# Performance work log

Measured on AMD Instinct MI355X. Metric: run time of the kernel, lower is better.

## Reference

```python
import jax, jax.numpy as jnp
import numpy as np

B, M, K, E, V, HOPS = 256, 128, 4, 512, 32000, 3


def setup_inputs() -> dict:
    key = jax.random.key(0)
    ks = jax.random.split(key, 12)

    def emb_table(k):
        t = 0.1 * jax.random.normal(k, (V, E), dtype=jnp.float32)
        return t.at[0].set(0.0)  # padding_idx=0

    inp = {
        "context": jax.random.randint(ks[0], (B, M, K), 0, V),
        "y_": jax.random.randint(ks[1], (B,), 0, V),
        "h_": jax.random.normal(ks[2], (1, B, E), dtype=jnp.float32),
        # embedding tables; C[i] tied to A[i+1], so distinct: A0,A1,A2,C2
        "A0": emb_table(ks[3]),
        "A1": emb_table(ks[4]),
        "A2": emb_table(ks[5]),
        "C2": emb_table(ks[6]),
        # GRU (single layer, single step): PyTorch layout [3E, E] and [3E]
        "W_ih": 0.05 * jax.random.normal(ks[7], (3 * E, E), dtype=jnp.float32),
        "W_hh": 0.05 * jax.random.normal(ks[8], (3 * E, E), dtype=jnp.float32),
        "b_ih": jnp.zeros((3 * E,), dtype=jnp.float32),
        "b_hh": jnp.zeros((3 * E,), dtype=jnp.float32),
        # lin_vocab: Linear(2E -> V)
        "lin_W": 0.02 * jax.random.normal(ks[9], (V, 2 * E), dtype=jnp.float32),
        "lin_b": jnp.zeros((V,), dtype=jnp.float32),
    }
    return inp


def _gru_step(x, h, W_ih, W_hh, b_ih, b_hh):
    gi = x @ W_ih.T + b_ih  # [B, 3E]
    gh = h @ W_hh.T + b_hh
    i_r, i_z, i_n = jnp.split(gi, 3, axis=-1)
    h_r, h_z, h_n = jnp.split(gh, 3, axis=-1)
    r = jax.nn.sigmoid(i_r + h_r)
    z = jax.nn.sigmoid(i_z + h_z)
    n = jnp.tanh(i_n + r * h_n)
    return (1.0 - z) * n + z * h


def reference(context, y_, h_, A0, A1, A2, C2, W_ih, W_hh, b_ih, b_hh, lin_W, lin_b):
    # memories[hop] = sum_k A[hop][context], memories[hops] = sum_k C[hops-1][context]
    tables = [A0, A1, A2, C2]
    memories = [t[context].sum(axis=2) for t in tables]  # each [B, M, E]

    m = A1[y_]  # C[0](y_) -- C[0].weight tied to A[1].weight, [B, E]
    h = _gru_step(m, h_[0], W_ih, W_hh, b_ih, b_hh)  # [B, E]

    q = h
    p = None
    p_vocab = None
    for hop in range(HOPS):
        p = jnp.einsum("bme,be->bm", memories[hop], q)  # dot-attention scores
        attn = jax.nn.softmax(p, axis=1)
        o = jnp.einsum("bm,bme->be", attn, memories[hop + 1])
        if hop == 0:
            p_vocab = jnp.concatenate([q, o], axis=1) @ lin_W.T + lin_b  # [B, V]
        q = q + o

    p_ptr = p  # last hop's pre-softmax scores [B, M]
    return (p_ptr, p_vocab, h[None])  # h: [1, B, E]
```

## Files before the change

kernel.cpp:

```cpp
#include <hip/hip_runtime.h>
#include <hip/hip_bf16.h>
#include <stdint.h>
#include <stddef.h>

#define Bb 256
#define Mm 128
#define Ee 512
#define Vv 32000
#define E3 1536

typedef __attribute__((ext_vector_type(8))) short bf16x8;
typedef __attribute__((ext_vector_type(4))) float f32x4;

__device__ __forceinline__ float bf2f(unsigned short u) {
  union { unsigned int i; float f; } v; v.i = ((unsigned int)u) << 16; return v.f;
}
__device__ __forceinline__ unsigned int f2bf(float f) {
  union { float f; unsigned int u; } v; v.f = f;
  unsigned int u = v.u;
  return ((u + 0x7fffu + ((u >> 16) & 1u)) >> 16);
}

__global__ void convert_kernel(const float* __restrict__ A0, const float* __restrict__ A1,
                               const float* __restrict__ A2,
                               unsigned short* __restrict__ tabB) {
  const int t = blockIdx.y;
  const float* src = (t == 0) ? A0 : (t == 1) ? A1 : A2;
  unsigned short* dst = tabB + (size_t)t * Vv * Ee;
  const int n4 = Vv * Ee / 4;
  for (int i = blockIdx.x * blockDim.x + threadIdx.x; i < n4; i += gridDim.x * blockDim.x) {
    f32x4 v = __builtin_nontemporal_load((const f32x4*)src + i);
    unsigned int o0 = f2bf(v.x) | (f2bf(v.y) << 16);
    unsigned int o1 = f2bf(v.z) | (f2bf(v.w) << 16);
    ((uint2*)dst)[i] = make_uint2(o0, o1);
  }
}

__global__ void gru_gemm_kernel(const int* __restrict__ y,
                                const float* __restrict__ A1,
                                const float* __restrict__ hprev,
                                const float* __restrict__ W_ih,
                                const float* __restrict__ W_hh,
                                float* __restrict__ gi,
                                float* __restrict__ gh) {
  const int z = blockIdx.z;
  const float* W = z ? W_hh : W_ih;
  float* C = z ? gh : gi;
  const int by = blockIdx.x * 64;
  const int jy = blockIdx.y * 64;
  __shared__ float As[16][65];
  __shared__ float Bs[16][65];
  const int tx = threadIdx.x & 15, ty = threadIdx.x >> 4;
  float acc[4][4] = {};
  for (int k0 = 0; k0 < Ee; k0 += 16) {
#pragma unroll
    for (int it = 0; it < 4; ++it) {
      int r = ty + it * 16;
      int row = by + r;
      const float* arow = z ? (hprev + (size_t)row * Ee) : (A1 + (size_t)y[row] * Ee);
      As[tx][r] = arow[k0 + tx];
      Bs[tx][r] = W[(size_t)(jy + r) * Ee + k0 + tx];
    }
    __syncthreads();
#pragma unroll
    for (int kk = 0; kk < 16; ++kk) {
      float a[4], bb[4];
#pragma unroll
      for (int i = 0; i < 4; ++i) { a[i] = As[kk][ty * 4 + i]; bb[i] = Bs[kk][tx * 4 + i]; }
#pragma unroll
      for (int i = 0; i < 4; ++i)
#pragma unroll
        for (int j = 0; j < 4; ++j)
          acc[i][j] += a[i] * bb[j];
    }
    __syncthreads();
  }
#pragma unroll
  for (int i = 0; i < 4; ++i)
#pragma unroll
    for (int j = 0; j < 4; ++j)
      C[(size_t)(by + ty * 4 + i) * E3 + jy + tx * 4 + j] = acc[i][j];
}

__global__ __launch_bounds__(1024) void fused_kernel(
    const int* __restrict__ ctx,
    const unsigned short* __restrict__ tabB,
    const float* __restrict__ A0, const float* __restrict__ A1,
    const float* __restrict__ A2,
    const float* __restrict__ gi, const float* __restrict__ gh,
    const float* __restrict__ b_ih, const float* __restrict__ b_hh,
    const float* __restrict__ h0,
    float* __restrict__ out_h, unsigned short* __restrict__ in2,
    float* __restrict__ p_out) {
  extern __shared__ char smem[];
  unsigned short* Vlds = (unsigned short*)smem;
  float* p_lds = (float*)(smem + 131072);
  float* qbuf = (float*)(smem + 131584);
  float* obuf = (float*)(smem + 133632);

  const int b = blockIdx.x;
  const int tid = threadIdx.x;
  const int lane = tid & 63, w = tid >> 6;

  if (tid < 512) {
    const int e = tid;
    const float* gib = gi + (size_t)b * E3;
    const float* ghb = gh + (size_t)b * E3;
    float ir = gib[e] + b_ih[e];
    float iz = gib[512 + e] + b_ih[512 + e];
    float inn = gib[1024 + e] + b_ih[1024 + e];
    float hr = ghb[e] + b_hh[e];
    float hz = ghb[512 + e] + b_hh[512 + e];
    float hn = ghb[1024 + e] + b_hh[1024 + e];
    float r = 1.f / (1.f + __expf(-(ir + hr)));
    float z = 1.f / (1.f + __expf(-(iz + hz)));
    float n = tanhf(inn + r * hn);
    float hp = h0[(size_t)b * Ee + e];
    float hnew = (1.f - z) * n + z * hp;
    out_h[(size_t)b * Ee + e] = hnew;
    in2[(size_t)b * 1024 + e] = (unsigned short)f2bf(hnew);
    qbuf[e] = hnew;
  }

#define GATHER_B(T)                                                          \
  {                                                                          \
    const unsigned short* Tb = tabB + (size_t)(T) * ((size_t)Vv * Ee);       \
    _Pragma("unroll 2")                                                      \
    for (int r8 = 0; r8 < 8; ++r8) {                                         \
      const int row = w * 8 + r8;                                            \
      const int4 cc = *(const int4*)(ctx + ((size_t)b * Mm + row) * 4);      \
      uint4 va = *(const uint4*)(Tb + (size_t)cc.x * Ee + lane * 8);         \
      uint4 vb = *(const uint4*)(Tb + (size_t)cc.y * Ee + lane * 8);         \
      uint4 vc = *(const uint4*)(Tb + (size_t)cc.z * Ee + lane * 8);         \
      uint4 vd = *(const uint4*)(Tb + (size_t)cc.w * Ee + lane * 8);         \
      const unsigned int* pa = (const unsigned int*)&va;                     \
      const unsigned int* pb = (const unsigned int*)&vb;                     \
      const unsigned int* pc = (const unsigned int*)&vc;                     \
      const unsigned int* pd = (const unsigned int*)&vd;                     \
      unsigned int o[4];                                                     \
      _Pragma("unroll")                                                      \
      for (int j = 0; j < 4; ++j) {                                          \
        float lo = bf2f((unsigned short)(pa[j] & 0xffff)) +                  \
                   bf2f((unsigned short)(pb[j] & 0xffff)) +                  \
                   bf2f((unsigned short)(pc[j] & 0xffff)) +                  \
                   bf2f((unsigned short)(pd[j] & 0xffff));                   \
        float hi = bf2f((unsigned short)(pa[j] >> 16)) +                     \
                   bf2f((unsigned short)(pb[j] >> 16)) +                     \
                   bf2f((unsigned short)(pc[j] >> 16)) +                     \
                   bf2f((unsigned short)(pd[j] >> 16));                      \
        o[j] = f2bf(lo) | (f2bf(hi) << 16);                                  \
      }                                                                      \
      *(uint4*)(Vlds + (size_t)row * Ee + lane * 8) = *(uint4*)o;            \
    }                                                                        \
  }

#define GATHER_F(TAB)                                                        \
  {                                                                          \
    _Pragma("unroll 2")                                                      \
    for (int r8 = 0; r8 < 8; ++r8) {                                         \
      const int row = w * 8 + r8;                                            \
      const int4 cc = *(const int4*)(ctx + ((size_t)b * Mm + row) * 4);      \
      const float* s0 = TAB + (size_t)cc.x * Ee + lane * 8;                  \
      const float* s1 = TAB + (size_t)cc.y * Ee + lane * 8;                  \
      const float* s2 = TAB + (size_t)cc.z * Ee + lane * 8;                  \
      const float* s3 = TAB + (size_t)cc.w * Ee + lane * 8;                  \
      float4 a0 = *(const float4*)s0, a1 = *(const float4*)(s0 + 4);         \
      float4 b0 = *(const float4*)s1, b1 = *(const float4*)(s1 + 4);         \
      float4 c0 = *(const float4*)s2, c1 = *(const float4*)(s2 + 4);         \
      float4 d0 = *(const float4*)s3, d1 = *(const float4*)(s3 + 4);         \
      unsigned int o[4];                                                     \
      o[0] = f2bf(a0.x + b0.x + c0.x + d0.x) |                               \
             (f2bf(a0.y + b0.y + c0.y + d0.y) << 16);                        \
      o[1] = f2bf(a0.z + b0.z + c0.z + d0.z) |                               \
             (f2bf(a0.w + b0.w + c0.w + d0.w) << 16);                        \
      o[2] = f2bf(a1.x + b1.x + c1.x + d1.x) |                               \
             (f2bf(a1.y + b1.y + c1.y + d1.y) << 16);                        \
      o[3] = f2bf(a1.z + b1.z + c1.z + d1.z) |                               \
             (f2bf(a1.w + b1.w + c1.w + d1.w) << 16);                        \
      *(uint4*)(Vlds + (size_t)row * Ee + lane * 8) = *(uint4*)o;            \
    }                                                                        \
  }

#define GATHER(T, TAB) { if (tabB) GATHER_B(T) else GATHER_F(TAB) }

#define SCORE_PHASE(EMIT)                                                    \
  {                                                                          \
    float qf[8];                                                             \
    *(float4*)&qf[0] = *(const float4*)&qbuf[lane * 8];                      \
    *(float4*)&qf[4] = *(const float4*)&qbuf[lane * 8 + 4];                  \
    _Pragma("unroll")                                                        \
    for (int r = 0; r < 8; ++r) {                                            \
      const int m = w * 8 + r;                                               \
      uint4 kv = *(const uint4*)(Vlds + (size_t)m * Ee + lane * 8);          \
      const unsigned int* p4 = (const unsigned int*)&kv;                     \
      float s = 0.f;                                                         \
      _Pragma("unroll")                                                      \
      for (int x = 0; x < 4; ++x) {                                          \
        s += bf2f((unsigned short)(p4[x] & 0xffff)) * qf[2 * x];             \
        s += bf2f((unsigned short)(p4[x] >> 16)) * qf[2 * x + 1];            \
      }                                                                      \
      _Pragma("unroll")                                                      \
      for (int off = 32; off > 0; off >>= 1) s += __shfl_down(s, off);       \
      if (lane == 0) { EMIT; }                                               \
    }                                                                        \
  }

#define SOFTMAX_PHASE                                                        \
  if (tid < 64) {                                                            \
    float v0 = p_lds[tid], v1 = p_lds[tid + 64];                             \
    float mx = fmaxf(v0, v1);                                                \
    _Pragma("unroll")                                                        \
    for (int off = 32; off > 0; off >>= 1) mx = fmaxf(mx, __shfl_xor(mx, off)); \
    float e0 = __expf(v0 - mx), e1 = __expf(v1 - mx);                        \
    float s = e0 + e1;                                                       \
    _Pragma("unroll")                                                        \
    for (int off = 32; off > 0; off >>= 1) s += __shfl_xor(s, off);          \
    float inv = 1.f / s;                                                     \
    p_lds[tid] = e0 * inv;                                                   \
    p_lds[tid + 64] = e1 * inv;                                              \
  }

#define O_PHASE                                                              \
  {                                                                          \
    const int g = tid >> 8, t = tid & 255;                                   \
    const int e2 = t * 2;                                                    \
    float a0 = 0.f, a1 = 0.f;                                                \
    _Pragma("unroll 4")                                                      \
    for (int m = g * 32; m < g * 32 + 32; ++m) {                             \
      unsigned int vv = *(const unsigned int*)(Vlds + (size_t)m * Ee + e2);  \
      float ww = p_lds[m];                                                   \
      a0 += ww * bf2f((unsigned short)(vv & 0xffff));                        \
      a1 += ww * bf2f((unsigned short)(vv >> 16));                           \
    }                                                                        \
    obuf[g * 512 + e2] = a0;                                                 \
    obuf[g * 512 + e2 + 1] = a1;                                             \
  }

  GATHER(0, A0)
  __syncthreads();
  SCORE_PHASE(p_lds[m] = s)
  __syncthreads();
  SOFTMAX_PHASE
  GATHER(1, A1)
  __syncthreads();
  O_PHASE
  __syncthreads();
  if (tid < 512) {
    const int e = tid;
    float o = obuf[e] + obuf[512 + e] + obuf[1024 + e] + obuf[1536 + e];
    qbuf[e] = qbuf[e] + o;
    in2[(size_t)b * 1024 + 512 + e] = (unsigned short)f2bf(o);
  }
  __syncthreads();

  SCORE_PHASE(p_lds[m] = s)
  __syncthreads();
  SOFTMAX_PHASE
  GATHER(2, A2)
  __syncthreads();
  O_PHASE
  __syncthreads();
  if (tid < 512) {
    const int e = tid;
    qbuf[e] = qbuf[e] + obuf[e] + obuf[512 + e] + obuf[1024 + e] + obuf[1536 + e];
  }
  __syncthreads();

  SCORE_PHASE(p_out[b * Mm + m] = s)
}

__global__ __launch_bounds__(512) void pvocab_kernel(
    const unsigned short* __restrict__ in2,
    const float* __restrict__ lin_W,
    const float* __restrict__ lin_b,
    float* __restrict__ out_pv) {
  const int v0 = blockIdx.x * 128;
  const int m0 = blockIdx.y * 128;
  const int tid = threadIdx.x;
  const int lane = tid & 63, w = tid >> 6;
  const int wm = w >> 2, wn = w & 3;
  const int l15 = lane & 15, lg = lane >> 4;
  __shared__ __align__(16) unsigned short As[128][64];
  __shared__ __align__(16) unsigned short Ws[128][64];

  f32x4 acc[4][2];
#pragma unroll
  for (int i = 0; i < 4; ++i)
#pragma unroll
    for (int j = 0; j < 2; ++j)
      acc[i][j] = (f32x4){0.f, 0.f, 0.f, 0.f};

  for (int k0 = 0; k0 < 1024; k0 += 64) {
    {
      const int u = tid & 7;
      const int rb = tid >> 3;
#pragma unroll
      for (int it = 0; it < 2; ++it) {
        int r = rb + it * 64;
        uint4 val = *(const uint4*)(in2 + (size_t)(m0 + r) * 1024 + k0 + u * 8);
        *(uint4*)(&As[r][((u + r) & 7) * 8]) = val;
      }
    }
    {
      const int c = tid & 15;
      const int rb = tid >> 4;
#pragma unroll
      for (int it = 0; it < 4; ++it) {
        int r = rb + it * 32;
        float4 wv = *(const float4*)(lin_W + (size_t)(v0 + r) * 1024 + k0 + c * 4);
        unsigned int o0 = f2bf(wv.x) | (f2bf(wv.y) << 16);
        unsigned int o1 = f2bf(wv.z) | (f2bf(wv.w) << 16);
        int u = c >> 1, h = c & 1;
        *(uint2*)(&Ws[r][((u + r) & 7) * 8 + h * 4]) = make_uint2(o0, o1);
      }
    }
    __syncthreads();
#pragma unroll
    for (int kk = 0; kk < 2; ++kk) {
      const int cu = kk * 4 + lg;
      bf16x8 wf[2], af[4];
#pragma unroll
      for (int j = 0; j < 2; ++j) {
        int row = wn * 32 + j * 16 + l15;
        wf[j] = *(const bf16x8*)(&Ws[row][((cu + row) & 7) * 8]);
      }
#pragma unroll
      for (int i = 0; i < 4; ++i) {
        int row = wm * 64 + i * 16 + l15;
        af[i] = *(const bf16x8*)(&As[row][((cu + row) & 7) * 8]);
      }
#pragma unroll
      for (int i = 0; i < 4; ++i)
#pragma unroll
        for (int j = 0; j < 2; ++j)
          acc[i][j] = __builtin_amdgcn_mfma_f32_16x16x32_bf16(af[i], wf[j], acc[i][j], 0, 0, 0);
    }
    __syncthreads();
  }

#pragma unroll
  for (int j = 0; j < 2; ++j) {
    int v = v0 + wn * 32 + j * 16 + l15;
    float bias = lin_b[v];
#pragma unroll
    for (int i = 0; i < 4; ++i) {
      int brow = m0 + wm * 64 + i * 16 + lg * 4;
#pragma unroll
      for (int rr = 0; rr < 4; ++rr)
        out_pv[(size_t)(brow + rr) * Vv + v] = acc[i][j][rr] + bias;
    }
  }
}

extern "C" void kernel_launch(void* const* d_in, const int* in_sizes, int n_in,
                              void* d_out, int out_size, void* d_ws, size_t ws_size,
                              hipStream_t stream) {
  const int* ctx = (const int*)d_in[0];
  const int* y = (const int*)d_in[1];
  const float* h0 = (const float*)d_in[2];
  const float* A0 = (const float*)d_in[3];
  const float* A1 = (const float*)d_in[4];
  const float* A2 = (const float*)d_in[5];
  const float* W_ih = (const float*)d_in[7];
  const float* W_hh = (const float*)d_in[8];
  const float* b_ih = (const float*)d_in[9];
  const float* b_hh = (const float*)d_in[10];
  const float* lin_W = (const float*)d_in[11];
  const float* lin_b = (const float*)d_in[12];

  const size_t tabBytes = (size_t)3 * Vv * Ee * 2;
  const size_t giBytes = (size_t)Bb * E3 * 4;
  const size_t in2Bytes = (size_t)Bb * 1024 * 2;
  const bool bf16path = ws_size >= tabBytes + 2 * giBytes + in2Bytes;

  char* ws = (char*)d_ws;
  size_t off = 0;
  unsigned short* tabB = nullptr;
  if (bf16path) { tabB = (unsigned short*)ws; off += tabBytes; }
  float* gi = (float*)(ws + off); off += giBytes;
  float* gh = (float*)(ws + off); off += giBytes;
  unsigned short* in2 = (unsigned short*)(ws + off);

  float* out = (float*)d_out;
  float* p_ptr = out;
  float* p_voc = out + Bb * Mm;
  float* out_h = out + Bb * Mm + (size_t)Bb * Vv;

  if (bf16path)
    convert_kernel<<<dim3(4096, 3), 256, 0, stream>>>(A0, A1, A2, tabB);
  gru_gemm_kernel<<<dim3(4, 24, 2), 256, 0, stream>>>(y, A1, h0, W_ih, W_hh, gi, gh);
  hipFuncSetAttribute((const void*)fused_kernel,
                      hipFuncAttributeMaxDynamicSharedMemorySize, 141824);
  fused_kernel<<<Bb, 1024, 141824, stream>>>(ctx, tabB, A0, A1, A2, gi, gh,
                                             b_ih, b_hh, h0, out_h, in2, p_ptr);
  pvocab_kernel<<<dim3(Vv / 128, 2), 512, 0, stream>>>(in2, lin_W, lin_b, p_voc);
}
```

Before: 231.0 us.

## Double-buffer LDS tiles with register prefetch in pvocab GEMM

```diff
diff --git a/kernel.cpp b/kernel.cpp
--- a/kernel.cpp
+++ b/kernel.cpp
@@ -280,8 +280,11 @@
   const int lane = tid & 63, w = tid >> 6;
   const int wm = w >> 2, wn = w & 3;
   const int l15 = lane & 15, lg = lane >> 4;
-  __shared__ __align__(16) unsigned short As[128][64];
-  __shared__ __align__(16) unsigned short Ws[128][64];
+  __shared__ __align__(16) unsigned short As[2][128][64];
+  __shared__ __align__(16) unsigned short Ws[2][128][64];
+
+  const int au = tid & 7, arb = tid >> 3;
+  const int wc = tid & 15, wrb = tid >> 4;
 
   f32x4 acc[4][2];
 #pragma unroll
@@ -290,31 +293,47 @@
     for (int j = 0; j < 2; ++j)
       acc[i][j] = (f32x4){0.f, 0.f, 0.f, 0.f};
 
-  for (int k0 = 0; k0 < 1024; k0 += 64) {
-    {
-      const int u = tid & 7;
-      const int rb = tid >> 3;
-#pragma unroll
-      for (int it = 0; it < 2; ++it) {
-        int r = rb + it * 64;
-        uint4 val = *(const uint4*)(in2 + (size_t)(m0 + r) * 1024 + k0 + u * 8);
-        *(uint4*)(&As[r][((u + r) & 7) * 8]) = val;
-      }
-    }
-    {
-      const int c = tid & 15;
-      const int rb = tid >> 4;
-#pragma unroll
-      for (int it = 0; it < 4; ++it) {
-        int r = rb + it * 32;
-        float4 wv = *(const float4*)(lin_W + (size_t)(v0 + r) * 1024 + k0 + c * 4);
-        unsigned int o0 = f2bf(wv.x) | (f2bf(wv.y) << 16);
-        unsigned int o1 = f2bf(wv.z) | (f2bf(wv.w) << 16);
-        int u = c >> 1, h = c & 1;
-        *(uint2*)(&Ws[r][((u + r) & 7) * 8 + h * 4]) = make_uint2(o0, o1);
-      }
-    }
-    __syncthreads();
+  uint4 aR[2];
+  float4 wR[4];
+
+#define PV_STAGE_LOAD(K0)                                                    \
+  {                                                                          \
+    _Pragma("unroll")                                                        \
+    for (int it = 0; it < 2; ++it) {                                         \
+      int r = arb + it * 64;                                                 \
+      aR[it] = *(const uint4*)(in2 + (size_t)(m0 + r) * 1024 + (K0) + au * 8); \
+    }                                                                        \
+    _Pragma("unroll")                                                        \
+    for (int it = 0; it < 4; ++it) {                                         \
+      int r = wrb + it * 32;                                                 \
+      wR[it] = *(const float4*)(lin_W + (size_t)(v0 + r) * 1024 + (K0) + wc * 4); \
+    }                                                                        \
+  }
+
+#define PV_STAGE_WRITE(BUF)                                                  \
+  {                                                                          \
+    _Pragma("unroll")                                                        \
+    for (int it = 0; it < 2; ++it) {                                         \
+      int r = arb + it * 64;                                                 \
+      *(uint4*)(&As[BUF][r][((au + r) & 7) * 8]) = aR[it];                   \
+    }                                                                        \
+    _Pragma("unroll")                                                        \
+    for (int it = 0; it < 4; ++it) {                                         \
+      int r = wrb + it * 32;                                                 \
+      unsigned int o0 = f2bf(wR[it].x) | (f2bf(wR[it].y) << 16);             \
+      unsigned int o1 = f2bf(wR[it].z) | (f2bf(wR[it].w) << 16);             \
+      int u = wc >> 1, h = wc & 1;                                           \
+      *(uint2*)(&Ws[BUF][r][((u + r) & 7) * 8 + h * 4]) = make_uint2(o0, o1); \
+    }                                                                        \
+  }
+
+  PV_STAGE_LOAD(0)
+  PV_STAGE_WRITE(0)
+  __syncthreads();
+
+  int cur = 0;
+  for (int t = 0; t < 16; ++t) {
+    if (t + 1 < 16) PV_STAGE_LOAD((t + 1) * 64)
 #pragma unroll
     for (int kk = 0; kk < 2; ++kk) {
       const int cu = kk * 4 + lg;
@@ -322,12 +341,12 @@
 #pragma unroll
       for (int j = 0; j < 2; ++j) {
         int row = wn * 32 + j * 16 + l15;
-        wf[j] = *(const bf16x8*)(&Ws[row][((cu + row) & 7) * 8]);
+        wf[j] = *(const bf16x8*)(&Ws[cur][row][((cu + row) & 7) * 8]);
       }
 #pragma unroll
       for (int i = 0; i < 4; ++i) {
         int row = wm * 64 + i * 16 + l15;
-        af[i] = *(const bf16x8*)(&As[row][((cu + row) & 7) * 8]);
+        af[i] = *(const bf16x8*)(&As[cur][row][((cu + row) & 7) * 8]);
       }
 #pragma unroll
       for (int i = 0; i < 4; ++i)
@@ -335,7 +354,11 @@
         for (int j = 0; j < 2; ++j)
           acc[i][j] = __builtin_amdgcn_mfma_f32_16x16x32_bf16(af[i], wf[j], acc[i][j], 0, 0, 0);
     }
-    __syncthreads();
+    if (t + 1 < 16) {
+      PV_STAGE_WRITE(cur ^ 1)
+      __syncthreads();
+      cur ^= 1;
+    }
   }
 
 #pragma unroll
```

After: 220.4 us. 1.05x faster.
